# Kernel tuning notes

Hardware: AMD Instinct MI355X
Metric: run time of the kernel (lower is better)

The kernel has to match this reference:

```python
import jax, jax.numpy as jnp
import numpy as np

# Dims: B=2, S=2048, D=1024 hidden, E=8 experts, F=2752 ffn (SwiGLU), top-1 gate,
# capacity_factor=1.0 -> capacity C = (B*S)//E = 512. Residual-MoE (moe_use_residual=True).

def setup_inputs() -> dict:
    key = jax.random.key(0)
    ks = jax.random.split(key, 10)
    B, S, D, E, F = 2, 2048, 1024, 8, 2752
    sc = 0.02
    return {
        "hidden_states": jax.random.normal(ks[0], (B, S, D), jnp.float32),
        "wg":  jax.random.normal(ks[1], (D, E), jnp.float32) * sc,   # gate
        "w1":  jax.random.normal(ks[2], (E, D, F), jnp.float32) * sc,  # expert SwiGLU
        "w3":  jax.random.normal(ks[3], (E, D, F), jnp.float32) * sc,
        "w2":  jax.random.normal(ks[4], (E, F, D), jnp.float32) * sc,
        "rw1": jax.random.normal(ks[5], (D, F), jnp.float32) * sc,    # residual MLP (SwiGLU, no bias)
        "rw3": jax.random.normal(ks[6], (D, F), jnp.float32) * sc,
        "rw2": jax.random.normal(ks[7], (F, D), jnp.float32) * sc,
        "cw":  jax.random.normal(ks[8], (D, 2), jnp.float32) * sc,    # coefficient Linear(D, 2)
        "cb":  jnp.zeros((2,), jnp.float32),
    }


def _moe_forward(x, wg, w1, w3, w2):
    """GShard/DeepSpeed-style top-1 gated MoE with capacity + token dropping.
    x: [T, D] flattened tokens. Returns (out [T,D], l_aux scalar, exp_counts [E])."""
    T, D = x.shape
    E = wg.shape[1]
    C = max(4, T // E)  # capacity_factor = 1.0, min_capacity = 4

    logits = x @ wg                                  # [T, E]
    gates = jax.nn.softmax(logits, axis=-1)
    idx = jnp.argmax(gates, axis=-1)                 # top-1 expert per token
    mask1 = jax.nn.one_hot(idx, E, dtype=gates.dtype)  # [T, E]
    exp_counts = jnp.sum(mask1, axis=0).astype(jnp.int32)

    # load-balancing aux loss (DeepSpeed top1gating)
    me = jnp.mean(gates, axis=0)
    ce = jnp.mean(mask1, axis=0)
    l_aux = jnp.sum(me * ce) * E

    # position of each token within its expert's buffer; drop overflow
    locations = jnp.cumsum(mask1, axis=0) - 1.0      # [T, E]
    mask1 = mask1 * (locations < C)
    loc_s = jnp.sum(locations * mask1, axis=1).astype(jnp.int32)  # [T]
    gates1 = jnp.sum(gates * mask1, axis=1)          # [T] gate weight (0 if dropped)

    loc_oh = jax.nn.one_hot(loc_s, C, dtype=gates.dtype)          # [T, C]
    combine = gates1[:, None, None] * mask1[:, :, None] * loc_oh[:, None, :]  # [T, E, C]
    dispatch = (combine > 0).astype(x.dtype)

    xe = jnp.einsum("tec,td->ecd", dispatch, x)      # dispatch to [E, C, D]
    h = jax.nn.silu(jnp.einsum("ecd,edf->ecf", xe, w1)) * jnp.einsum("ecd,edf->ecf", xe, w3)
    ye = jnp.einsum("ecf,efd->ecd", h, w2)           # expert SwiGLU FFN
    out = jnp.einsum("tec,ecd->td", combine, ye)     # weighted combine back to tokens
    return out, l_aux, exp_counts


def reference(hidden_states, wg, w1, w3, w2, rw1, rw3, rw2, cw, cb):
    B, S, D = hidden_states.shape
    x = hidden_states.reshape(-1, D)
    moe_out, l_aux, exp_counts = _moe_forward(x, wg, w1, w3, w2)
    moe_out = moe_out.reshape(B, S, D)

    # residual SwiGLU MLP + softmax-gated combine (Residual-MoE)
    mlp = (jax.nn.silu(hidden_states @ rw1) * (hidden_states @ rw3)) @ rw2
    coef = jax.nn.softmax(hidden_states @ cw + cb, axis=-1)  # [B, S, 2]
    output = moe_out * coef[..., 0:1] + mlp * coef[..., 1:2]
    return output, l_aux, exp_counts
```

## Files before the change

kernel.cpp:

```cpp
#include <hip/hip_runtime.h>
#include <hip/hip_bf16.h>
#include <stdint.h>

#define T_TOK 4096
#define DD 1024
#define EE 8
#define CC 512
#define FF 2752

typedef __attribute__((ext_vector_type(8))) short bf16x8;
typedef __attribute__((ext_vector_type(4))) float f32x4;
typedef __attribute__((ext_vector_type(4))) unsigned short us4;
typedef __attribute__((ext_vector_type(8))) unsigned short us8;

__device__ __forceinline__ float bf2f(unsigned short u) {
  union { float f; unsigned int i; } v; v.i = ((unsigned int)u) << 16; return v.f;
}
__device__ __forceinline__ unsigned short f2bf(float f) {
  union { float f; unsigned int i; } v; v.f = f;
  unsigned int r = v.i + 0x7fffu + ((v.i >> 16) & 1u);
  return (unsigned short)(r >> 16);
}

#define GLDS16(g, l) __builtin_amdgcn_global_load_lds( \
    (const __attribute__((address_space(1))) void*)(g), \
    (__attribute__((address_space(3))) void*)(l), 16, 0, 0)

#define STG_CHUNK(l) (((l & 3) ^ ((l >> 3) & 3)) * 8)
#define RD_OFF(fr, fq) ((fr) * 32 + (((fq) ^ (((fr) >> 1) & 3)) * 8))

#define BAR() do { asm volatile("" ::: "memory"); __builtin_amdgcn_s_barrier(); \
                   asm volatile("" ::: "memory"); } while (0)

__global__ __launch_bounds__(256)
void transpose_k(const float* __restrict__ in, const float* __restrict__ in2,
                 unsigned short* __restrict__ out, unsigned short* __restrict__ out2,
                 int R, int C, long inStride, long outStride, float* __restrict__ me) {
  __shared__ float smf[64][65];
  int b = blockIdx.z;
  if (b == 0 && blockIdx.x == 0 && blockIdx.y == 0 && threadIdx.x < EE)
    me[threadIdx.x] = 0.0f;
  if (b < EE) { in += (long)b * inStride; out += (long)b * outStride; }
  else { in = in2; out = out2; }
  int cb = blockIdx.x * 64, rb = blockIdx.y * 64;
  int t = threadIdx.x;
  int rr = t >> 4, c4 = (t & 15) * 4;
#pragma unroll
  for (int i = 0; i < 4; ++i) {
    int r = rr + i * 16;
    float4 v = *(const float4*)(in + (long)(rb + r) * C + cb + c4);
    smf[c4 + 0][r] = v.x;
    smf[c4 + 1][r] = v.y;
    smf[c4 + 2][r] = v.z;
    smf[c4 + 3][r] = v.w;
  }
  __syncthreads();
#pragma unroll
  for (int j = 0; j < 2; ++j) {
    int idx = t + j * 256;
    int g = idx & 7, c = idx >> 3;
    int r8 = g * 8;
    us8 o;
#pragma unroll
    for (int k = 0; k < 8; ++k) o[k] = f2bf(smf[c][r8 + k]);
    *(us8*)(out + (long)(cb + c) * R + rb + r8) = o;
  }
}

__global__ void gate_k(const float* __restrict__ x, const float* __restrict__ wg,
                       const float* __restrict__ cw, const float* __restrict__ cbv,
                       int* __restrict__ idx, float* __restrict__ gatev,
                       float* __restrict__ coef, float* __restrict__ me_sum) {
  int tid = threadIdx.x, lane = tid & 63, wv = tid >> 6;
  int t = blockIdx.x * 4 + wv;
  const float* xr = x + (long)t * DD;
  float acc[EE] = {0,0,0,0,0,0,0,0};
  float c0 = 0.0f, c1 = 0.0f;
  for (int d = lane; d < DD; d += 64) {
    float xv = xr[d];
#pragma unroll
    for (int e = 0; e < EE; ++e) acc[e] += xv * wg[d * EE + e];
    c0 += xv * cw[d * 2 + 0];
    c1 += xv * cw[d * 2 + 1];
  }
#pragma unroll
  for (int o = 32; o > 0; o >>= 1) {
#pragma unroll
    for (int e = 0; e < EE; ++e) acc[e] += __shfl_xor(acc[e], o);
    c0 += __shfl_xor(c0, o);
    c1 += __shfl_xor(c1, o);
  }
  __shared__ float sme[EE];
  if (tid < EE) sme[tid] = 0.0f;
  __syncthreads();
  if (lane == 0) {
    float m = acc[0]; int am = 0;
#pragma unroll
    for (int e = 1; e < EE; ++e) if (acc[e] > m) { m = acc[e]; am = e; }
    float g[EE]; float s = 0.0f;
#pragma unroll
    for (int e = 0; e < EE; ++e) { g[e] = __expf(acc[e] - m); s += g[e]; }
    float inv = 1.0f / s;
    idx[t] = am;
    gatev[t] = g[am] * inv;
#pragma unroll
    for (int e = 0; e < EE; ++e) atomicAdd(&sme[e], g[e] * inv);
    float l0 = c0 + cbv[0], l1 = c1 + cbv[1];
    float mm = fmaxf(l0, l1);
    float e0 = __expf(l0 - mm), e1 = __expf(l1 - mm);
    float is = 1.0f / (e0 + e1);
    coef[t * 2 + 0] = e0 * is;
    coef[t * 2 + 1] = e1 * is;
  }
  __syncthreads();
  if (tid < EE) atomicAdd(&me_sum[tid], sme[tid]);
}

__global__ void scan_k(const int* __restrict__ idx, const float* __restrict__ me_sum,
                       int* __restrict__ slot, int* __restrict__ tok,
                       float* __restrict__ out_tail) {
  __shared__ int sidx[T_TOK];
  __shared__ int counts[EE];
  int tid = threadIdx.x;
  for (int i = tid; i < T_TOK; i += 512) sidx[i] = idx[i];
  __syncthreads();
  int e = tid >> 6, lane = tid & 63;
  int base = 0;
  for (int it = 0; it < T_TOK / 64; ++it) {
    int t = it * 64 + lane;
    bool f = (sidx[t] == e);
    unsigned long long m = __ballot(f);
    if (f) {
      int loc = base + __popcll(m & ((1ull << lane) - 1ull));
      slot[t] = (loc < CC) ? loc : -1;
      if (loc < CC) tok[e * CC + loc] = t;
    }
    base += __popcll(m);
  }
  if (lane == 0) counts[e] = base;
  __syncthreads();
  int filled = min(counts[e], CC);
  for (int c = filled + lane; c < CC; c += 64) tok[e * CC + c] = -1;
  if (tid == 0) {
    float la = 0.0f;
    for (int i = 0; i < EE; ++i) la += me_sum[i] * (float)counts[i];
    la *= (float)EE / ((float)T_TOK * (float)T_TOK);
    out_tail[0] = la;
    for (int i = 0; i < EE; ++i) out_tail[1 + i] = (float)counts[i];
  }
}

__global__ void gather_k(const float* __restrict__ x, const int* __restrict__ tok,
                         unsigned short* __restrict__ xb, unsigned short* __restrict__ xe) {
  int r = blockIdx.x, tid = threadIdx.x;
  int d = tid * 4;
  if (r < T_TOK) {
    float4 v = *(const float4*)(x + (long)r * DD + d);
    us4 o; o.x = f2bf(v.x); o.y = f2bf(v.y); o.z = f2bf(v.z); o.w = f2bf(v.w);
    *(us4*)(xb + (long)r * DD + d) = o;
  } else {
    int s = r - T_TOK;
    int t = tok[s];
    us4 o = {0, 0, 0, 0};
    if (t >= 0) {
      float4 v = *(const float4*)(x + (long)t * DD + d);
      o.x = f2bf(v.x); o.y = f2bf(v.y); o.z = f2bf(v.z); o.w = f2bf(v.w);
    }
    *(us4*)(xe + (long)s * DD + d) = o;
  }
}

__global__ __launch_bounds__(512, 2)
void gemm1_k(const unsigned short* __restrict__ xcat,
             const float* __restrict__ w1, const float* __restrict__ w3,
             const float* __restrict__ rw1, const float* __restrict__ rw3,
             unsigned short* __restrict__ Hcat) {
  int lin = blockIdx.x;
  int work = (lin & 7) * 88 + (lin >> 3);
  int mtile, ntile;
  if (work < 352) {
    int e = work / 44, r = work - e * 44;
    ntile = r >> 1;
    mtile = e * 2 + (r & 1);
  } else {
    int q = work - 352;
    ntile = q >> 4;
    mtile = 16 + (q & 15);
  }
  const unsigned short* A = xcat + (size_t)mtile * 256 * DD;
  const float *B1, *B3;
  if (mtile < 16) { int e = mtile >> 1; B1 = w1 + (size_t)e * DD * FF; B3 = w3 + (size_t)e * DD * FF; }
  else { B1 = rw1; B3 = rw3; }
  unsigned short* H = Hcat + (size_t)mtile * 256 * FF;
  int n0 = ntile * 128;

  __shared__ __align__(16) char Lc[147456];
  const unsigned short* ldsS = (const unsigned short*)Lc;

  int tid = threadIdx.x, l = tid & 63, w = tid >> 6;
  int wm = w >> 2, wn = w & 3;
  int fr = l & 15, fq = l >> 4;
  int srow = l >> 2, soff = STG_CHUNK(l);
  int rdo = RD_OFF(fr, fq);

  const unsigned short* gA0 = A + (size_t)(w * 16 + srow) * DD + soff;
  const unsigned short* gA1 = A + (size_t)((8 + w) * 16 + srow) * DD + soff;
  int lrow = l >> 5;
  int kl0 = 2 * w + lrow;
  int kl1 = 16 + 2 * w + lrow;
  int cs0 = (l & 31) ^ (((kl0 >> 3) & 1) << 2);
  int cs1 = (l & 31) ^ (((kl1 >> 3) & 1) << 2);
  int nn0 = n0 + 4 * cs0; if (nn0 >= FF) nn0 = 0;
  int nn1 = n0 + 4 * cs1; if (nn1 >= FF) nn1 = 0;
  const float* gB1a = B1 + (size_t)kl0 * FF + nn0;
  const float* gB1b = B1 + (size_t)kl1 * FF + nn1;
  const float* gB3a = B3 + (size_t)kl0 * FF + nn0;
  const float* gB3b = B3 + (size_t)kl1 * FF + nn1;

  int cb2[2][4];
#pragma unroll
  for (int ni = 0; ni < 2; ++ni) {
    int base = fq * 4096 + ((((wn * 2 + ni) * 64 + fr * 4)) ^ ((fq & 1) << 6));
#pragma unroll
    for (int p = 0; p < 4; ++p) cb2[ni][p] = base + p * 1024;
  }

#define STG1(bb, hw) do { size_t ka = (size_t)(hw) * 32; size_t kb = ka * FF;   \
    GLDS16(gA0 + ka, Lc + (bb) * 16384 + w * 1024);                             \
    GLDS16(gA1 + ka, Lc + (bb) * 16384 + (8 + w) * 1024);                       \
    GLDS16(gB1a + kb, Lc + 49152 + (bb) * 16384 + w * 1024);                    \
    GLDS16(gB1b + kb, Lc + 49152 + (bb) * 16384 + (8 + w) * 1024);              \
    GLDS16(gB3a + kb, Lc + 98304 + (bb) * 16384 + w * 1024);                    \
    GLDS16(gB3b + kb, Lc + 98304 + (bb) * 16384 + (8 + w) * 1024); } while (0)

  f32x4 acc1[8][2] = {};
  f32x4 acc3[8][2] = {};

  const int HN = 32;
  STG1(0, 0);
  STG1(1, 1);

  for (int h = 0; h < HN; ++h) {
    int buf = h % 3;
    int hw = h + 2; if (hw >= HN) hw -= HN;
    int bufw = (buf + 2) % 3;

    asm volatile("s_waitcnt vmcnt(6)" ::: "memory");
    BAR();
    STG1(bufw, hw);

    const char* Bb1 = Lc + 49152 + buf * 16384;
    const char* Bb3 = Lc + 98304 + buf * 16384;
    bf16x8 af[8];
#pragma unroll
    for (int mi = 0; mi < 8; ++mi)
      af[mi] = *(const bf16x8*)(ldsS + buf * 8192 + (wm * 8 + mi) * 512 + rdo);

    {
      float fb[2][8];
#pragma unroll
      for (int ni = 0; ni < 2; ++ni)
#pragma unroll
        for (int p = 0; p < 4; ++p) {
          const char* bp = Bb1 + cb2[ni][p];
          fb[ni][2 * p]     = *(const float*)(bp);
          fb[ni][2 * p + 1] = *(const float*)(bp + 512);
        }
      __builtin_amdgcn_s_setprio(1);
#pragma unroll
      for (int ni = 0; ni < 2; ++ni) {
        union { bf16x8 h; unsigned int u[4]; } bu;
#pragma unroll
        for (int p = 0; p < 4; ++p)
          asm("v_cvt_pk_bf16_f32 %0, %1, %2" : "=v"(bu.u[p]) : "v"(fb[ni][2 * p]), "v"(fb[ni][2 * p + 1]));
#pragma unroll
        for (int mi = 0; mi < 8; ++mi)
          acc1[mi][ni] = __builtin_amdgcn_mfma_f32_16x16x32_bf16(af[mi], bu.h, acc1[mi][ni], 0, 0, 0);
      }
      __builtin_amdgcn_s_setprio(0);
    }
    {
      float fb[2][8];
#pragma unroll
      for (int ni = 0; ni < 2; ++ni)
#pragma unroll
        for (int p = 0; p < 4; ++p) {
          const char* bp = Bb3 + cb2[ni][p];
          fb[ni][2 * p]     = *(const float*)(bp);
          fb[ni][2 * p + 1] = *(const float*)(bp + 512);
        }
      __builtin_amdgcn_s_setprio(1);
#pragma unroll
      for (int ni = 0; ni < 2; ++ni) {
        union { bf16x8 h; unsigned int u[4]; } bu;
#pragma unroll
        for (int p = 0; p < 4; ++p)
          asm("v_cvt_pk_bf16_f32 %0, %1, %2" : "=v"(bu.u[p]) : "v"(fb[ni][2 * p]), "v"(fb[ni][2 * p + 1]));
#pragma unroll
        for (int mi = 0; mi < 8; ++mi)
          acc3[mi][ni] = __builtin_amdgcn_mfma_f32_16x16x32_bf16(af[mi], bu.h, acc3[mi][ni], 0, 0, 0);
      }
      __builtin_amdgcn_s_setprio(0);
    }
  }
#undef STG1

#pragma unroll
  for (int mi = 0; mi < 8; ++mi)
#pragma unroll
    for (int ni = 0; ni < 2; ++ni)
#pragma unroll
      for (int r = 0; r < 4; ++r) {
        int gm = wm * 128 + mi * 16 + fq * 4 + r;
        int gn = n0 + (wn * 2 + ni) * 16 + fr;
        if (gn < FF) {
          float v1 = acc1[mi][ni][r], v3 = acc3[mi][ni][r];
          float h = v1 / (1.0f + __expf(-v1)) * v3;
          H[(size_t)gm * FF + gn] = f2bf(h);
        }
      }
}

__global__ __launch_bounds__(512, 2)
void gemm2_k(const unsigned short* __restrict__ Hcat,
             const unsigned short* __restrict__ w2t, const unsigned short* __restrict__ rw2t,
             unsigned short* __restrict__ Ycat) {
  int lin = blockIdx.x;
  int work = (lin & 7) * 32 + (lin >> 3);
  int mtile, ntile;
  if (work < 128) {
    int e = work >> 4, r = work & 15;
    ntile = r >> 1;
    mtile = e * 2 + (r & 1);
  } else {
    int q = work - 128;
    ntile = q >> 4;
    mtile = 16 + (q & 15);
  }
  const unsigned short* A = Hcat + (size_t)mtile * 256 * FF;
  const unsigned short* B = (mtile < 16) ? (w2t + (size_t)(mtile >> 1) * (size_t)DD * FF) : rw2t;
  unsigned short* Y = Ycat + (size_t)mtile * 256 * DD;
  int n0 = ntile * 128;

  __shared__ __align__(16) unsigned short lds[73728];
  char* Lc = (char*)lds;

  int tid = threadIdx.x, l = tid & 63, w = tid >> 6;
  int wm = w >> 1, wn = w & 1;
  int fr = l & 15, fq = l >> 4;
  int srow = l >> 2, soff = STG_CHUNK(l);
  int rdo = RD_OFF(fr, fq);

  const unsigned short* gA0 = A + (size_t)(w * 16 + srow) * FF + soff;
  const unsigned short* gA1 = A + (size_t)((8 + w) * 16 + srow) * FF + soff;
  const unsigned short* gB  = B + (size_t)(n0 + w * 16 + srow) * FF + soff;

#define STG2(bb, kk) do {                                          \
    GLDS16(gA0 + (kk), Lc + (bb) * 16384 + w * 1024);              \
    GLDS16(gA1 + (kk), Lc + (bb) * 16384 + (8 + w) * 1024);        \
    GLDS16(gB  + (kk), Lc + 98304 + (bb) * 8192 + w * 1024); } while (0)

  f32x4 acc[4][4] = {};

  const int HN = 86;
#pragma unroll
  for (int hh = 0; hh < 5; ++hh) STG2(hh, hh * 32);

  int b = 0;
#pragma unroll 2
  for (int h = 0; h < HN; ++h) {
    int bn = b ? b - 1 : 5;
    int hw = h + 5; if (hw >= HN) hw -= HN;
    int kk = hw * 32;
    bf16x8 af[4], bf[4];

    asm volatile("s_waitcnt vmcnt(12)" ::: "memory");
    BAR();
    STG2(bn, kk);
#pragma unroll
    for (int mi = 0; mi < 4; ++mi)
      af[mi] = *(const bf16x8*)(lds + b * 8192 + (wm * 4 + mi) * 512 + rdo);
#pragma unroll
    for (int ni = 0; ni < 4; ++ni)
      bf[ni] = *(const bf16x8*)(lds + 49152 + b * 4096 + (wn * 4 + ni) * 512 + rdo);
    __builtin_amdgcn_s_setprio(1);
#pragma unroll
    for (int mi = 0; mi < 4; ++mi)
#pragma unroll
      for (int ni = 0; ni < 4; ++ni)
        acc[mi][ni] = __builtin_amdgcn_mfma_f32_16x16x32_bf16(af[mi], bf[ni], acc[mi][ni], 0, 0, 0);
    __builtin_amdgcn_s_setprio(0);

    ++b; if (b == 6) b = 0;
  }
#undef STG2

#pragma unroll
  for (int mi = 0; mi < 4; ++mi)
#pragma unroll
    for (int ni = 0; ni < 4; ++ni)
#pragma unroll
      for (int r = 0; r < 4; ++r) {
        int gm = wm * 64 + mi * 16 + fq * 4 + r;
        int gn = n0 + wn * 64 + ni * 16 + fr;
        Y[(size_t)gm * DD + gn] = f2bf(acc[mi][ni][r]);
      }
}

__global__ void combine_k(const unsigned short* __restrict__ Ye, const unsigned short* __restrict__ Yr,
                          const int* __restrict__ idx, const int* __restrict__ slot,
                          const float* __restrict__ gatev, const float* __restrict__ coef,
                          float* __restrict__ out) {
  int t = blockIdx.x, tid = threadIdx.x;
  int d = tid * 4;
  float c0 = coef[t * 2], c1 = coef[t * 2 + 1];
  int s = slot[t];
  float g = gatev[t] * c0;
  us4 vr = *(const us4*)(Yr + (size_t)t * DD + d);
  float4 o;
  if (s >= 0) {
    us4 ve = *(const us4*)(Ye + ((size_t)idx[t] * CC + s) * DD + d);
    o.x = g * bf2f(ve.x) + c1 * bf2f(vr.x);
    o.y = g * bf2f(ve.y) + c1 * bf2f(vr.y);
    o.z = g * bf2f(ve.z) + c1 * bf2f(vr.z);
    o.w = g * bf2f(ve.w) + c1 * bf2f(vr.w);
  } else {
    o.x = c1 * bf2f(vr.x);
    o.y = c1 * bf2f(vr.y);
    o.z = c1 * bf2f(vr.z);
    o.w = c1 * bf2f(vr.w);
  }
  *(float4*)(out + (size_t)t * DD + d) = o;
}

extern "C" void kernel_launch(void* const* d_in, const int* in_sizes, int n_in,
                              void* d_out, int out_size, void* d_ws, size_t ws_size,
                              hipStream_t stream) {
  const float* x   = (const float*)d_in[0];
  const float* wg  = (const float*)d_in[1];
  const float* w1  = (const float*)d_in[2];
  const float* w3  = (const float*)d_in[3];
  const float* w2  = (const float*)d_in[4];
  const float* rw1 = (const float*)d_in[5];
  const float* rw3 = (const float*)d_in[6];
  const float* rw2 = (const float*)d_in[7];
  const float* cw  = (const float*)d_in[8];
  const float* cbv = (const float*)d_in[9];
  float* out = (float*)d_out;

  char* ws = (char*)d_ws;
  size_t o = 0;
  auto alloc = [&](size_t bytes) -> char* {
    char* p = ws + o; o = (o + bytes + 255) & ~(size_t)255; return p;
  };
  unsigned short* w2t  = (unsigned short*)alloc((size_t)EE * DD * FF * 2);
  unsigned short* rw2t = (unsigned short*)alloc((size_t)DD * FF * 2);
  unsigned short* xe   = (unsigned short*)alloc((size_t)T_TOK * DD * 2);
  unsigned short* xb   = (unsigned short*)alloc((size_t)T_TOK * DD * 2);
  unsigned short* He   = (unsigned short*)alloc((size_t)T_TOK * FF * 2);
  unsigned short* Hr   = (unsigned short*)alloc((size_t)T_TOK * FF * 2);
  unsigned short* Ye   = (unsigned short*)alloc((size_t)T_TOK * DD * 2);
  unsigned short* Yr   = (unsigned short*)alloc((size_t)T_TOK * DD * 2);
  int*   idxp  = (int*)alloc(T_TOK * 4);
  float* gatev = (float*)alloc(T_TOK * 4);
  int*   slotp = (int*)alloc(T_TOK * 4);
  int*   tokp  = (int*)alloc(EE * CC * 4);
  float* coefp = (float*)alloc(T_TOK * 2 * 4);
  float* mep   = (float*)alloc(256);
  if (o > ws_size) return;

  transpose_k<<<dim3(16, 43, EE + 1), 256, 0, stream>>>(w2, rw2, w2t, rw2t, FF, DD, (long)FF * DD, (long)DD * FF, mep);

  gate_k<<<T_TOK / 4, 256, 0, stream>>>(x, wg, cw, cbv, idxp, gatev, coefp, mep);
  scan_k<<<1, 512, 0, stream>>>(idxp, mep, slotp, tokp, out + (size_t)T_TOK * DD);
  gather_k<<<2 * T_TOK, 256, 0, stream>>>(x, tokp, xb, xe);
  gemm1_k<<<704, 512, 0, stream>>>(xe, w1, w3, rw1, rw3, He);
  gemm2_k<<<256, 512, 0, stream>>>(He, w2t, rw2t, Ye);
  combine_k<<<T_TOK, 256, 0, stream>>>(Ye, Yr, idxp, slotp, gatev, coefp, out);
}
```

Baseline: 261.9 us.

## Fold w2 transpose into gemm1 launch as extra blocks

```diff
diff --git a/kernel.cpp b/kernel.cpp
--- a/kernel.cpp
+++ b/kernel.cpp
@@ -32,40 +32,7 @@
 #define BAR() do { asm volatile("" ::: "memory"); __builtin_amdgcn_s_barrier(); \
                    asm volatile("" ::: "memory"); } while (0)
 
-__global__ __launch_bounds__(256)
-void transpose_k(const float* __restrict__ in, const float* __restrict__ in2,
-                 unsigned short* __restrict__ out, unsigned short* __restrict__ out2,
-                 int R, int C, long inStride, long outStride, float* __restrict__ me) {
-  __shared__ float smf[64][65];
-  int b = blockIdx.z;
-  if (b == 0 && blockIdx.x == 0 && blockIdx.y == 0 && threadIdx.x < EE)
-    me[threadIdx.x] = 0.0f;
-  if (b < EE) { in += (long)b * inStride; out += (long)b * outStride; }
-  else { in = in2; out = out2; }
-  int cb = blockIdx.x * 64, rb = blockIdx.y * 64;
-  int t = threadIdx.x;
-  int rr = t >> 4, c4 = (t & 15) * 4;
-#pragma unroll
-  for (int i = 0; i < 4; ++i) {
-    int r = rr + i * 16;
-    float4 v = *(const float4*)(in + (long)(rb + r) * C + cb + c4);
-    smf[c4 + 0][r] = v.x;
-    smf[c4 + 1][r] = v.y;
-    smf[c4 + 2][r] = v.z;
-    smf[c4 + 3][r] = v.w;
-  }
-  __syncthreads();
-#pragma unroll
-  for (int j = 0; j < 2; ++j) {
-    int idx = t + j * 256;
-    int g = idx & 7, c = idx >> 3;
-    int r8 = g * 8;
-    us8 o;
-#pragma unroll
-    for (int k = 0; k < 8; ++k) o[k] = f2bf(smf[c][r8 + k]);
-    *(us8*)(out + (long)(cb + c) * R + rb + r8) = o;
-  }
-}
+__global__ void zero_me_k(float* me) { if (threadIdx.x < EE) me[threadIdx.x] = 0.0f; }
 
 __global__ void gate_k(const float* __restrict__ x, const float* __restrict__ wg,
                        const float* __restrict__ cw, const float* __restrict__ cbv,
@@ -174,8 +141,46 @@
 void gemm1_k(const unsigned short* __restrict__ xcat,
              const float* __restrict__ w1, const float* __restrict__ w3,
              const float* __restrict__ rw1, const float* __restrict__ rw3,
-             unsigned short* __restrict__ Hcat) {
+             unsigned short* __restrict__ Hcat,
+             const float* __restrict__ w2, const float* __restrict__ rw2,
+             unsigned short* __restrict__ w2t, unsigned short* __restrict__ rw2t) {
+  __shared__ __align__(16) char Lc[147456];
   int lin = blockIdx.x;
+  int tid = threadIdx.x;
+
+  if (lin >= 704) {
+    int half = tid >> 8, t = tid & 255;
+    int tile = (lin - 704) * 2 + half;
+    int z = tile / 688, rem = tile - z * 688;
+    int y = rem >> 4, xb = rem & 15;
+    const float* tin = (z < EE) ? (w2 + (size_t)z * FF * DD) : rw2;
+    unsigned short* tout = (z < EE) ? (w2t + (size_t)z * DD * FF) : rw2t;
+    float* smf = (float*)(Lc + half * 17152);
+    int cbx = xb * 64, rb = y * 64;
+    int rr = t >> 4, c4 = (t & 15) * 4;
+#pragma unroll
+    for (int i = 0; i < 4; ++i) {
+      int r = rr + i * 16;
+      float4 v = *(const float4*)(tin + (size_t)(rb + r) * DD + cbx + c4);
+      smf[(c4 + 0) * 65 + r] = v.x;
+      smf[(c4 + 1) * 65 + r] = v.y;
+      smf[(c4 + 2) * 65 + r] = v.z;
+      smf[(c4 + 3) * 65 + r] = v.w;
+    }
+    __syncthreads();
+#pragma unroll
+    for (int j = 0; j < 2; ++j) {
+      int idx = t + j * 256;
+      int g = idx & 7, c = idx >> 3;
+      int r8 = g * 8;
+      us8 o;
+#pragma unroll
+      for (int k = 0; k < 8; ++k) o[k] = f2bf(smf[c * 65 + r8 + k]);
+      *(us8*)(tout + (size_t)(cbx + c) * FF + rb + r8) = o;
+    }
+    return;
+  }
+
   int work = (lin & 7) * 88 + (lin >> 3);
   int mtile, ntile;
   if (work < 352) {
@@ -194,10 +199,9 @@
   unsigned short* H = Hcat + (size_t)mtile * 256 * FF;
   int n0 = ntile * 128;
 
-  __shared__ __align__(16) char Lc[147456];
   const unsigned short* ldsS = (const unsigned short*)Lc;
 
-  int tid = threadIdx.x, l = tid & 63, w = tid >> 6;
+  int l = tid & 63, w = tid >> 6;
   int wm = w >> 2, wn = w & 3;
   int fr = l & 15, fq = l >> 4;
   int srow = l >> 2, soff = STG_CHUNK(l);
@@ -469,12 +473,11 @@
   float* mep   = (float*)alloc(256);
   if (o > ws_size) return;
 
-  transpose_k<<<dim3(16, 43, EE + 1), 256, 0, stream>>>(w2, rw2, w2t, rw2t, FF, DD, (long)FF * DD, (long)DD * FF, mep);
-
+  zero_me_k<<<1, 64, 0, stream>>>(mep);
   gate_k<<<T_TOK / 4, 256, 0, stream>>>(x, wg, cw, cbv, idxp, gatev, coefp, mep);
   scan_k<<<1, 512, 0, stream>>>(idxp, mep, slotp, tokp, out + (size_t)T_TOK * DD);
   gather_k<<<2 * T_TOK, 256, 0, stream>>>(x, tokp, xb, xe);
-  gemm1_k<<<704, 512, 0, stream>>>(xe, w1, w3, rw1, rw3, He);
+  gemm1_k<<<704 + 3096, 512, 0, stream>>>(xe, w1, w3, rw1, rw3, He, w2, rw2, w2t, rw2t);
   gemm2_k<<<256, 512, 0, stream>>>(He, w2t, rw2t, Ye);
   combine_k<<<T_TOK, 256, 0, stream>>>(Ye, Yr, idxp, slotp, gatev, coefp, out);
 }
```

After: 258.1 us. Within noise of the previous version (-1.4%).

## Fuse w2 fp32-to-bf16 conversion into gemm2 and drop transpose kernel

Applied to the files above, without the earlier changes.

```diff
diff --git a/kernel.cpp b/kernel.cpp
--- a/kernel.cpp
+++ b/kernel.cpp
@@ -32,40 +32,7 @@
 #define BAR() do { asm volatile("" ::: "memory"); __builtin_amdgcn_s_barrier(); \
                    asm volatile("" ::: "memory"); } while (0)
 
-__global__ __launch_bounds__(256)
-void transpose_k(const float* __restrict__ in, const float* __restrict__ in2,
-                 unsigned short* __restrict__ out, unsigned short* __restrict__ out2,
-                 int R, int C, long inStride, long outStride, float* __restrict__ me) {
-  __shared__ float smf[64][65];
-  int b = blockIdx.z;
-  if (b == 0 && blockIdx.x == 0 && blockIdx.y == 0 && threadIdx.x < EE)
-    me[threadIdx.x] = 0.0f;
-  if (b < EE) { in += (long)b * inStride; out += (long)b * outStride; }
-  else { in = in2; out = out2; }
-  int cb = blockIdx.x * 64, rb = blockIdx.y * 64;
-  int t = threadIdx.x;
-  int rr = t >> 4, c4 = (t & 15) * 4;
-#pragma unroll
-  for (int i = 0; i < 4; ++i) {
-    int r = rr + i * 16;
-    float4 v = *(const float4*)(in + (long)(rb + r) * C + cb + c4);
-    smf[c4 + 0][r] = v.x;
-    smf[c4 + 1][r] = v.y;
-    smf[c4 + 2][r] = v.z;
-    smf[c4 + 3][r] = v.w;
-  }
-  __syncthreads();
-#pragma unroll
-  for (int j = 0; j < 2; ++j) {
-    int idx = t + j * 256;
-    int g = idx & 7, c = idx >> 3;
-    int r8 = g * 8;
-    us8 o;
-#pragma unroll
-    for (int k = 0; k < 8; ++k) o[k] = f2bf(smf[c][r8 + k]);
-    *(us8*)(out + (long)(cb + c) * R + rb + r8) = o;
-  }
-}
+__global__ void zero_me_k(float* me) { if (threadIdx.x < EE) me[threadIdx.x] = 0.0f; }
 
 __global__ void gate_k(const float* __restrict__ x, const float* __restrict__ wg,
                        const float* __restrict__ cw, const float* __restrict__ cbv,
@@ -323,7 +290,7 @@
 
 __global__ __launch_bounds__(512, 2)
 void gemm2_k(const unsigned short* __restrict__ Hcat,
-             const unsigned short* __restrict__ w2t, const unsigned short* __restrict__ rw2t,
+             const float* __restrict__ w2, const float* __restrict__ rw2,
              unsigned short* __restrict__ Ycat) {
   int lin = blockIdx.x;
   int work = (lin & 7) * 32 + (lin >> 3);
@@ -338,71 +305,98 @@
     mtile = 16 + (q & 15);
   }
   const unsigned short* A = Hcat + (size_t)mtile * 256 * FF;
-  const unsigned short* B = (mtile < 16) ? (w2t + (size_t)(mtile >> 1) * (size_t)DD * FF) : rw2t;
+  const float* B = (mtile < 16) ? (w2 + (size_t)(mtile >> 1) * (size_t)FF * DD) : rw2;
   unsigned short* Y = Ycat + (size_t)mtile * 256 * DD;
   int n0 = ntile * 128;
 
-  __shared__ __align__(16) unsigned short lds[73728];
-  char* Lc = (char*)lds;
+  __shared__ __align__(16) char Lc[98304];
+  const unsigned short* ldsS = (const unsigned short*)Lc;
 
   int tid = threadIdx.x, l = tid & 63, w = tid >> 6;
-  int wm = w >> 1, wn = w & 1;
+  int wm = w >> 2, wn = w & 3;
   int fr = l & 15, fq = l >> 4;
   int srow = l >> 2, soff = STG_CHUNK(l);
   int rdo = RD_OFF(fr, fq);
 
   const unsigned short* gA0 = A + (size_t)(w * 16 + srow) * FF + soff;
   const unsigned short* gA1 = A + (size_t)((8 + w) * 16 + srow) * FF + soff;
-  const unsigned short* gB  = B + (size_t)(n0 + w * 16 + srow) * FF + soff;
-
-#define STG2(bb, kk) do {                                          \
-    GLDS16(gA0 + (kk), Lc + (bb) * 16384 + w * 1024);              \
-    GLDS16(gA1 + (kk), Lc + (bb) * 16384 + (8 + w) * 1024);        \
-    GLDS16(gB  + (kk), Lc + 98304 + (bb) * 8192 + w * 1024); } while (0)
-
-  f32x4 acc[4][4] = {};
+  int lrow = l >> 5;
+  int kl0 = 2 * w + lrow;
+  int kl1 = 16 + 2 * w + lrow;
+  int cs0 = (l & 31) ^ (((kl0 >> 3) & 1) << 2);
+  int cs1 = (l & 31) ^ (((kl1 >> 3) & 1) << 2);
+  int nn0 = n0 + 4 * cs0;
+  int nn1 = n0 + 4 * cs1;
+  const float* gBa = B + (size_t)kl0 * DD + nn0;
+  const float* gBb = B + (size_t)kl1 * DD + nn1;
+
+  int cb2[2][4];
+#pragma unroll
+  for (int ni = 0; ni < 2; ++ni) {
+    int base = fq * 4096 + ((((wn * 2 + ni) * 64 + fr * 4)) ^ ((fq & 1) << 6));
+#pragma unroll
+    for (int p = 0; p < 4; ++p) cb2[ni][p] = base + p * 1024;
+  }
+
+#define STG2(bb, hw) do { size_t ka = (size_t)(hw) * 32; size_t kb = ka * DD;   \
+    GLDS16(gA0 + ka, Lc + (bb) * 16384 + w * 1024);                             \
+    GLDS16(gA1 + ka, Lc + (bb) * 16384 + (8 + w) * 1024);                       \
+    GLDS16(gBa + kb, Lc + 49152 + (bb) * 16384 + w * 1024);                     \
+    GLDS16(gBb + kb, Lc + 49152 + (bb) * 16384 + (8 + w) * 1024); } while (0)
+
+  f32x4 acc[8][2] = {};
 
   const int HN = 86;
-#pragma unroll
-  for (int hh = 0; hh < 5; ++hh) STG2(hh, hh * 32);
-
-  int b = 0;
-#pragma unroll 2
+  STG2(0, 0);
+  STG2(1, 1);
+
   for (int h = 0; h < HN; ++h) {
-    int bn = b ? b - 1 : 5;
-    int hw = h + 5; if (hw >= HN) hw -= HN;
-    int kk = hw * 32;
-    bf16x8 af[4], bf[4];
-
-    asm volatile("s_waitcnt vmcnt(12)" ::: "memory");
+    int buf = h % 3;
+    int hw = h + 2; if (hw >= HN) hw -= HN;
+    int bufw = (buf + 2) % 3;
+
+    asm volatile("s_waitcnt vmcnt(4)" ::: "memory");
     BAR();
-    STG2(bn, kk);
-#pragma unroll
-    for (int mi = 0; mi < 4; ++mi)
-      af[mi] = *(const bf16x8*)(lds + b * 8192 + (wm * 4 + mi) * 512 + rdo);
-#pragma unroll
-    for (int ni = 0; ni < 4; ++ni)
-      bf[ni] = *(const bf16x8*)(lds + 49152 + b * 4096 + (wn * 4 + ni) * 512 + rdo);
+    STG2(bufw, hw);
+
+    const char* Bb = Lc + 49152 + buf * 16384;
+    bf16x8 af[8];
+#pragma unroll
+    for (int mi = 0; mi < 8; ++mi)
+      af[mi] = *(const bf16x8*)(ldsS + buf * 8192 + (wm * 8 + mi) * 512 + rdo);
+
+    float fb[2][8];
+#pragma unroll
+    for (int ni = 0; ni < 2; ++ni)
+#pragma unroll
+      for (int p = 0; p < 4; ++p) {
+        const char* bp = Bb + cb2[ni][p];
+        fb[ni][2 * p]     = *(const float*)(bp);
+        fb[ni][2 * p + 1] = *(const float*)(bp + 512);
+      }
     __builtin_amdgcn_s_setprio(1);
 #pragma unroll
-    for (int mi = 0; mi < 4; ++mi)
-#pragma unroll
-      for (int ni = 0; ni < 4; ++ni)
-        acc[mi][ni] = __builtin_amdgcn_mfma_f32_16x16x32_bf16(af[mi], bf[ni], acc[mi][ni], 0, 0, 0);
+    for (int ni = 0; ni < 2; ++ni) {
+      union { bf16x8 h; unsigned int u[4]; } bu;
+#pragma unroll
+      for (int p = 0; p < 4; ++p)
+        asm("v_cvt_pk_bf16_f32 %0, %1, %2" : "=v"(bu.u[p]) : "v"(fb[ni][2 * p]), "v"(fb[ni][2 * p + 1]));
+#pragma unroll
+      for (int mi = 0; mi < 8; ++mi)
+        acc[mi][ni] = __builtin_amdgcn_mfma_f32_16x16x32_bf16(af[mi], bu.h, acc[mi][ni], 0, 0, 0);
+    }
     __builtin_amdgcn_s_setprio(0);
-
-    ++b; if (b == 6) b = 0;
   }
 #undef STG2
 
 #pragma unroll
-  for (int mi = 0; mi < 4; ++mi)
-#pragma unroll
-    for (int ni = 0; ni < 4; ++ni)
+  for (int mi = 0; mi < 8; ++mi)
+#pragma unroll
+    for (int ni = 0; ni < 2; ++ni)
 #pragma unroll
       for (int r = 0; r < 4; ++r) {
-        int gm = wm * 64 + mi * 16 + fq * 4 + r;
-        int gn = n0 + wn * 64 + ni * 16 + fr;
+        int gm = wm * 128 + mi * 16 + fq * 4 + r;
+        int gn = n0 + (wn * 2 + ni) * 16 + fr;
         Y[(size_t)gm * DD + gn] = f2bf(acc[mi][ni][r]);
       }
 }
@@ -453,8 +447,6 @@
   auto alloc = [&](size_t bytes) -> char* {
     char* p = ws + o; o = (o + bytes + 255) & ~(size_t)255; return p;
   };
-  unsigned short* w2t  = (unsigned short*)alloc((size_t)EE * DD * FF * 2);
-  unsigned short* rw2t = (unsigned short*)alloc((size_t)DD * FF * 2);
   unsigned short* xe   = (unsigned short*)alloc((size_t)T_TOK * DD * 2);
   unsigned short* xb   = (unsigned short*)alloc((size_t)T_TOK * DD * 2);
   unsigned short* He   = (unsigned short*)alloc((size_t)T_TOK * FF * 2);
@@ -469,12 +461,11 @@
   float* mep   = (float*)alloc(256);
   if (o > ws_size) return;
 
-  transpose_k<<<dim3(16, 43, EE + 1), 256, 0, stream>>>(w2, rw2, w2t, rw2t, FF, DD, (long)FF * DD, (long)DD * FF, mep);
-
+  zero_me_k<<<1, 64, 0, stream>>>(mep);
   gate_k<<<T_TOK / 4, 256, 0, stream>>>(x, wg, cw, cbv, idxp, gatev, coefp, mep);
   scan_k<<<1, 512, 0, stream>>>(idxp, mep, slotp, tokp, out + (size_t)T_TOK * DD);
   gather_k<<<2 * T_TOK, 256, 0, stream>>>(x, tokp, xb, xe);
   gemm1_k<<<704, 512, 0, stream>>>(xe, w1, w3, rw1, rw3, He);
-  gemm2_k<<<256, 512, 0, stream>>>(He, w2t, rw2t, Ye);
+  gemm2_k<<<256, 512, 0, stream>>>(He, w2, rw2, Ye);
   combine_k<<<T_TOK, 256, 0, stream>>>(Ye, Yr, idxp, slotp, gatev, coefp, out);
 }
```

Result: faster. 255.4 us (-2.5%).
